# Optimization experiments

Measured on AMD Instinct MI355X. Metric: run time of the kernel, lower is better.

The kernel has to match this reference:

```python
import jax, jax.numpy as jnp
import numpy as np


def setup_inputs() -> dict:
    key = jax.random.key(0)
    ks = jax.random.split(key, 12)
    L, B, T, E, H = 8, 256, 8, 1024, 1024
    w_scale = 1.0 / np.sqrt(E + H)  # keep gates out of saturation (mimics Linear init scale)
    inp = {
        "x": jax.random.normal(ks[0], (B, T, E), dtype=jnp.float32),
        "h0": jax.random.normal(ks[1], (L, B, H), dtype=jnp.float32),
        "c0": jax.random.normal(ks[2], (L, B, H), dtype=jnp.float32),
        "Wu": jax.random.normal(ks[3], (L, E + H, H), dtype=jnp.float32) * w_scale,
        "bu": jax.random.normal(ks[4], (L, H), dtype=jnp.float32) * w_scale,
        "Wf": jax.random.normal(ks[5], (L, E + H, H), dtype=jnp.float32) * w_scale,
        "bf": jax.random.normal(ks[6], (L, H), dtype=jnp.float32) * w_scale,
        "Wo": jax.random.normal(ks[7], (L, E + H, H), dtype=jnp.float32) * w_scale,
        "bo": jax.random.normal(ks[8], (L, H), dtype=jnp.float32) * w_scale,
        "Wc": jax.random.normal(ks[9], (L, E + H, H), dtype=jnp.float32) * w_scale,
        "bc": jax.random.normal(ks[10], (L, H), dtype=jnp.float32) * w_scale,
    }
    return inp


def reference(x, h0, c0, Wu, bu, Wf, bf, Wo, bo, Wc, bc):
    # x: [B,T,E]; h0,c0: [L,B,H]; W*: [L,E+H,H]; b*: [L,H]
    # Faithful to source: num_cells layers, time loop over first num_cells steps (T == L here).
    L = h0.shape[0]
    h = jnp.transpose(h0, (1, 0, 2))  # [B,L,H]
    c = jnp.transpose(c0, (1, 0, 2))

    def step(carry, xt):  # xt: [B,E]
        h, c = carry
        inp = xt
        hs, cs = [], []
        for l in range(L):
            zh = jnp.concatenate([inp, h[:, l]], axis=-1)  # [B, E+H]
            u = jax.nn.sigmoid(zh @ Wu[l] + bu[l])
            f = jax.nn.sigmoid(zh @ Wf[l] + bf[l])
            o = jax.nn.sigmoid(zh @ Wo[l] + bo[l])
            c_tilde = jnp.tanh(zh @ Wc[l] + bc[l])
            c_new = f * c[:, l] + u * c_tilde
            h_new = o * jnp.tanh(c_new)
            hs.append(h_new)
            cs.append(c_new)
            inp = h_new
        h = jnp.stack(hs, axis=1)
        c = jnp.stack(cs, axis=1)
        return (h, c), (h_new, c_new)  # emit top-layer h_t, c_t

    (_, _), (hs, cs) = jax.lax.scan(step, (h, c), jnp.transpose(x, (1, 0, 2)))
    hidden_states = jnp.transpose(hs, (1, 0, 2))  # [B,T,H]
    memory_states = jnp.transpose(cs, (1, 0, 2))
    h_t = hidden_states[:, -1:, :]  # [B,1,H], matches torch slice-shape
    c_t = memory_states[:, -1:, :]
    return hidden_states, memory_states, h_t, c_t
```

## Files before the change

kernel.cpp:

```cpp
#include <hip/hip_runtime.h>
#include <hip/hip_bf16.h>

#define B_ 256
#define T_ 8
#define E_ 1024
#define H_ 1024
#define L_ 8
#define KD 2048
#define ND 4096

#define BM 256
#define BN 128
#define BK 64
#define ABYTES 32768
#define BUFBYTES 49152

typedef __bf16 bf16x8 __attribute__((ext_vector_type(8)));
typedef float floatx4 __attribute__((ext_vector_type(4)));

struct bh4 { __hip_bfloat16 x, y, z, w; };

__device__ __forceinline__ float sigm(float x) { return 1.f / (1.f + __expf(-x)); }
__device__ __forceinline__ float tanh_(float x) { return 1.f - 2.f / (__expf(2.f * x) + 1.f); }

__device__ __forceinline__ void async16(const void* g, void* l) {
    __builtin_amdgcn_global_load_lds(
        (const __attribute__((address_space(1))) void*)g,
        (__attribute__((address_space(3))) void*)l, 16, 0, 0);
}

__global__ __launch_bounds__(256) void prep_weights(
    const float* __restrict__ Wu, const float* __restrict__ Wf,
    const float* __restrict__ Wo, const float* __restrict__ Wc,
    __hip_bfloat16* __restrict__ WT)
{
    __shared__ float sm[32][33];
    int bid = blockIdx.x;
    int jt = bid & 31;
    int kt = (bid >> 5) & 63;
    int g  = (bid >> 11) & 3;
    int l  = bid >> 13;
    const float* src = (g == 0) ? Wu : (g == 1) ? Wf : (g == 2) ? Wo : Wc;
    int tid = threadIdx.x;
    int jl = tid & 31;
    int kl0 = tid >> 5;
#pragma unroll
    for (int r = 0; r < 4; ++r) {
        int kl = r * 8 + kl0;
        sm[kl][jl] = src[((size_t)(l * KD + kt * 32 + kl)) * 1024 + jt * 32 + jl];
    }
    __syncthreads();
    int jw = tid >> 3;
    int kc = (tid & 7) * 4;
    bh4 v;
    v.x = __float2bfloat16(sm[kc + 0][jw]);
    v.y = __float2bfloat16(sm[kc + 1][jw]);
    v.z = __float2bfloat16(sm[kc + 2][jw]);
    v.w = __float2bfloat16(sm[kc + 3][jw]);
    size_t n = (size_t)(jt * 32 + jw) * 4 + g;
    *(bh4*)&WT[((size_t)l * ND + n) * KD + kt * 32 + kc] = v;
}

__global__ __launch_bounds__(256) void prep_misc(
    const float* __restrict__ x,  const float* __restrict__ h0,
    const float* __restrict__ c0,
    const float* __restrict__ bu, const float* __restrict__ bfv,
    const float* __restrict__ bo, const float* __restrict__ bc,
    __hip_bfloat16* __restrict__ xbf, __hip_bfloat16* __restrict__ hb0,
    float* __restrict__ cbuf, float* __restrict__ bcat)
{
    size_t i = (size_t)blockIdx.x * 256 + threadIdx.x;
    const size_t NX = (size_t)B_ * T_ * E_;
    const size_t NH = (size_t)L_ * B_ * H_;
    if (i < NX) {
        xbf[i] = __float2bfloat16(x[i]);
    } else if (i < NX + NH) {
        size_t j = i - NX; hb0[j] = __float2bfloat16(h0[j]);
    } else if (i < NX + 2 * NH) {
        size_t j = i - NX - NH; cbuf[j] = c0[j];
    } else if (i < NX + 2 * NH + (size_t)L_ * ND) {
        size_t j = i - NX - 2 * NH;
        int l = (int)(j >> 12); int n = (int)(j & 4095);
        int jj = n >> 2; int g = n & 3;
        const float* bs = (g == 0) ? bu : (g == 1) ? bfv : (g == 2) ? bo : bc;
        bcat[j] = bs[l * 1024 + jj];
    }
}

__global__ __launch_bounds__(512) void lstm_step(
    int d, int tmin,
    const __hip_bfloat16* __restrict__ xbf,
    const __hip_bfloat16* __restrict__ WT,
    const float* __restrict__ bcat,
    __hip_bfloat16* __restrict__ hb0,
    __hip_bfloat16* __restrict__ hb1,
    float* __restrict__ cbuf,
    float* __restrict__ out)
{
    __shared__ __align__(16) char smraw[2][BUFBYTES];

    int cell = blockIdx.x >> 5;
    int nb   = blockIdx.x & 31;
    int t = tmin + cell;
    int l = d - t;

    const __hip_bfloat16* hread  = (t & 1) ? hb1 : hb0;
    __hip_bfloat16*       hwrite = (t & 1) ? hb0 : hb1;

    const __hip_bfloat16* A1; int sA1;
    if (l == 0) { A1 = xbf + (size_t)t * E_;               sA1 = T_ * E_; }
    else        { A1 = hwrite + (size_t)(l - 1) * B_ * H_; sA1 = H_; }
    const __hip_bfloat16* A2 = hread + (size_t)l * B_ * H_;
    const __hip_bfloat16* Bbase = WT + ((size_t)l * ND + (size_t)nb * BN) * KD;

    int tid  = threadIdx.x;
    int lane = tid & 63;
    int wid  = tid >> 6;
    int wm = (wid & 3) * 64;
    int wn = (wid >> 2) * 64;
    int lr   = lane & 15;
    int quad = lane >> 4;

    int srow = tid >> 3;
    int c    = (tid & 7) ^ (srow & 7);
    const __hip_bfloat16* pA1[4];
    const __hip_bfloat16* pA2[4];
    const __hip_bfloat16* pB[2];
#pragma unroll
    for (int s = 0; s < 4; ++s) {
        int row = s * 64 + srow;
        pA1[s] = A1 + (size_t)row * sA1 + c * 8;
        pA2[s] = A2 + (size_t)row * H_ + c * 8 - E_;
    }
#pragma unroll
    for (int s = 0; s < 2; ++s) {
        int row = s * 64 + srow;
        pB[s] = Bbase + (size_t)row * KD + c * 8;
    }
    int ldsWaveOff = wid * 1024;

    auto stage = [&](int k0, int buf) {
        char* dst = smraw[buf];
        bool first = (k0 < E_);
#pragma unroll
        for (int s = 0; s < 4; ++s) {
            const __hip_bfloat16* g = (first ? pA1[s] : pA2[s]) + k0;
            async16(g, dst + s * 8192 + ldsWaveOff);
        }
#pragma unroll
        for (int s = 0; s < 2; ++s) {
            async16(pB[s] + k0, dst + ABYTES + s * 8192 + ldsWaveOff);
        }
    };

    floatx4 acc[4][4];
    floatx4 zero = {0.f, 0.f, 0.f, 0.f};
#pragma unroll
    for (int mi = 0; mi < 4; ++mi)
#pragma unroll
        for (int ni = 0; ni < 4; ++ni) acc[mi][ni] = zero;

    stage(0, 0);
    __syncthreads();

    for (int kt = 0; kt < KD / BK; ++kt) {
        int cur = kt & 1;
        if (kt < KD / BK - 1) stage((kt + 1) * BK, cur ^ 1);

        const __hip_bfloat16* sm = (const __hip_bfloat16*)smraw[cur];
        const __hip_bfloat16* smB = sm + ABYTES / 2;
#pragma unroll
        for (int ks = 0; ks < 2; ++ks) {
            int xo = (((ks * 4 + quad) ^ (lr & 7)) * 8);
            bf16x8 af[4], bfr[4];
#pragma unroll
            for (int mi = 0; mi < 4; ++mi)
                af[mi] = *(const bf16x8*)&sm[(wm + mi * 16 + lr) * 64 + xo];
#pragma unroll
            for (int ni = 0; ni < 4; ++ni)
                bfr[ni] = *(const bf16x8*)&smB[(wn + ni * 16 + lr) * 64 + xo];
#pragma unroll
            for (int mi = 0; mi < 4; ++mi)
#pragma unroll
                for (int ni = 0; ni < 4; ++ni)
                    acc[mi][ni] = __builtin_amdgcn_mfma_f32_16x16x32_bf16(
                        af[mi], bfr[ni], acc[mi][ni], 0, 0, 0);
        }
        __syncthreads();
    }

    float* outH  = out;
    float* outC  = out + (size_t)B_ * T_ * H_;
    float* outHt = out + 2 * (size_t)B_ * T_ * H_;
    float* outCt = outHt + (size_t)B_ * H_;
    auto sC = (float(*)[BN + 4])smraw[0];

    for (int q = 0; q < 4; ++q) {
        __syncthreads();
        if ((wid & 3) == q) {
#pragma unroll
            for (int mi = 0; mi < 4; ++mi)
#pragma unroll
                for (int ni = 0; ni < 4; ++ni)
#pragma unroll
                    for (int r = 0; r < 4; ++r)
                        sC[mi * 16 + quad * 4 + r][wn + ni * 16 + lr] = acc[mi][ni][r];
        }
        __syncthreads();
#pragma unroll
        for (int s = 0; s < 4; ++s) {
            int p = tid + s * 512;
            int r  = p >> 5;
            int jj = p & 31;
            float4 v  = *(float4*)&sC[r][jj * 4];
            float4 bb = *(const float4*)&bcat[(size_t)l * ND + nb * BN + jj * 4];
            float u  = sigm(v.x + bb.x);
            float f  = sigm(v.y + bb.y);
            float o  = sigm(v.z + bb.z);
            float ct = tanh_(v.w + bb.w);
            int b = q * 64 + r;
            int j = nb * 32 + jj;
            size_t ci = ((size_t)l * B_ + b) * H_ + j;
            float cn = f * cbuf[ci] + u * ct;
            cbuf[ci] = cn;
            float hn = o * tanh_(cn);
            hwrite[ci] = __float2bfloat16(hn);
            if (l == L_ - 1) {
                size_t oi = ((size_t)b * T_ + t) * H_ + j;
                outH[oi] = hn;
                outC[oi] = cn;
                if (t == T_ - 1) {
                    outHt[(size_t)b * H_ + j] = hn;
                    outCt[(size_t)b * H_ + j] = cn;
                }
            }
        }
    }
}

extern "C" void kernel_launch(void* const* d_in, const int* in_sizes, int n_in,
                              void* d_out, int out_size, void* d_ws, size_t ws_size,
                              hipStream_t stream)
{
    const float* x   = (const float*)d_in[0];
    const float* h0  = (const float*)d_in[1];
    const float* c0  = (const float*)d_in[2];
    const float* Wu  = (const float*)d_in[3];
    const float* bu  = (const float*)d_in[4];
    const float* Wf  = (const float*)d_in[5];
    const float* bfv = (const float*)d_in[6];
    const float* Wo  = (const float*)d_in[7];
    const float* bo  = (const float*)d_in[8];
    const float* Wc  = (const float*)d_in[9];
    const float* bc  = (const float*)d_in[10];
    float* out = (float*)d_out;

    char* ws = (char*)d_ws;
    __hip_bfloat16* WT   = (__hip_bfloat16*)(ws);
    float*          bcat = (float*)(ws + 134217728);
    __hip_bfloat16* xbf  = (__hip_bfloat16*)(ws + 134348800);
    __hip_bfloat16* hb0  = (__hip_bfloat16*)(ws + 138543104);
    __hip_bfloat16* hb1  = (__hip_bfloat16*)(ws + 142737408);
    float*          cbuf = (float*)(ws + 146931712);

    hipLaunchKernelGGL(prep_weights, dim3(65536), dim3(256), 0, stream,
                       Wu, Wf, Wo, Wc, WT);
    size_t n2 = (size_t)2097152 * 3 + (size_t)L_ * ND;
    hipLaunchKernelGGL(prep_misc, dim3((unsigned)((n2 + 255) / 256)), dim3(256), 0, stream,
                       x, h0, c0, bu, bfv, bo, bc, xbf, hb0, cbuf, bcat);

    for (int dg = 0; dg <= (T_ - 1) + (L_ - 1); ++dg) {
        int tmin = dg > L_ - 1 ? dg - (L_ - 1) : 0;
        int tmax = dg < T_ - 1 ? dg : T_ - 1;
        int nc = tmax - tmin + 1;
        hipLaunchKernelGGL(lstm_step, dim3(nc * 32), dim3(512), 0, stream,
                           dg, tmin, xbf, WT, bcat, hb0, hb1, cbuf, out);
    }
}
```

Measured before the change: 966.3 us.

## Register-staged double-buffer GEMM pipeline and wider tiles in weight prep

The GEMM main loop stops using direct global-to-LDS async loads. It now prefetches two K-tiles ahead into registers, writes them to the alternate LDS buffer after compute, and synchronises with an explicit lgkmcnt wait plus a barrier. This is meant to hide global latency across a full compute phase and drop the per-iteration __syncthreads over vmcnt. Separately, the weight transpose/convert kernel moves to 64x64 tiles with float4 loads and 16-byte bf16 stores, using fewer, larger blocks. The trade-off is higher register pressure (12 uint4 staging registers plus the accumulators) and extra LDS write instructions. The hand-written waitcnt also relies on global loads finishing before the LDS writes that consume them.

```diff
diff --git a/kernel.cpp b/kernel.cpp
--- a/kernel.cpp
+++ b/kernel.cpp
@@ -12,53 +12,52 @@
 #define BM 256
 #define BN 128
 #define BK 64
+#define KT (KD / BK)
 #define ABYTES 32768
 #define BUFBYTES 49152
 
+#define WAITCNT_LGKM0 0xC07F
+
 typedef __bf16 bf16x8 __attribute__((ext_vector_type(8)));
 typedef float floatx4 __attribute__((ext_vector_type(4)));
 
-struct bh4 { __hip_bfloat16 x, y, z, w; };
-
 __device__ __forceinline__ float sigm(float x) { return 1.f / (1.f + __expf(-x)); }
 __device__ __forceinline__ float tanh_(float x) { return 1.f - 2.f / (__expf(2.f * x) + 1.f); }
-
-__device__ __forceinline__ void async16(const void* g, void* l) {
-    __builtin_amdgcn_global_load_lds(
-        (const __attribute__((address_space(1))) void*)g,
-        (__attribute__((address_space(3))) void*)l, 16, 0, 0);
-}
 
 __global__ __launch_bounds__(256) void prep_weights(
     const float* __restrict__ Wu, const float* __restrict__ Wf,
     const float* __restrict__ Wo, const float* __restrict__ Wc,
     __hip_bfloat16* __restrict__ WT)
 {
-    __shared__ float sm[32][33];
+    __shared__ float sm[64][65];
     int bid = blockIdx.x;
-    int jt = bid & 31;
-    int kt = (bid >> 5) & 63;
-    int g  = (bid >> 11) & 3;
-    int l  = bid >> 13;
+    int jt = bid & 15;
+    int kt = (bid >> 4) & 31;
+    int g  = (bid >> 9) & 3;
+    int l  = bid >> 11;
     const float* src = (g == 0) ? Wu : (g == 1) ? Wf : (g == 2) ? Wo : Wc;
     int tid = threadIdx.x;
-    int jl = tid & 31;
-    int kl0 = tid >> 5;
-#pragma unroll
-    for (int r = 0; r < 4; ++r) {
-        int kl = r * 8 + kl0;
-        sm[kl][jl] = src[((size_t)(l * KD + kt * 32 + kl)) * 1024 + jt * 32 + jl];
+    int cr = tid >> 4;
+    int cc = (tid & 15) * 4;
+    const float* base = src + ((size_t)(l * KD + kt * 64)) * 1024 + jt * 64;
+#pragma unroll
+    for (int p = 0; p < 4; ++p) {
+        int kr = p * 16 + cr;
+        float4 v = *(const float4*)(base + (size_t)kr * 1024 + cc);
+        sm[kr][cc] = v.x; sm[kr][cc + 1] = v.y; sm[kr][cc + 2] = v.z; sm[kr][cc + 3] = v.w;
     }
     __syncthreads();
-    int jw = tid >> 3;
-    int kc = (tid & 7) * 4;
-    bh4 v;
-    v.x = __float2bfloat16(sm[kc + 0][jw]);
-    v.y = __float2bfloat16(sm[kc + 1][jw]);
-    v.z = __float2bfloat16(sm[kc + 2][jw]);
-    v.w = __float2bfloat16(sm[kc + 3][jw]);
-    size_t n = (size_t)(jt * 32 + jw) * 4 + g;
-    *(bh4*)&WT[((size_t)l * ND + n) * KD + kt * 32 + kc] = v;
+    int kc8 = (tid & 7) * 8;
+    int jr0 = tid >> 3;
+#pragma unroll
+    for (int p = 0; p < 2; ++p) {
+        int jr = p * 32 + jr0;
+        __hip_bfloat16 tmp[8];
+#pragma unroll
+        for (int i = 0; i < 8; ++i) tmp[i] = __float2bfloat16(sm[kc8 + i][jr]);
+        size_t n = (size_t)(jt * 64 + jr) * 4 + g;
+        *(uint4*)&WT[((size_t)l * ND + n) * KD + kt * 64 + kc8] = *(uint4*)tmp;
+    }
 }
 
 __global__ __launch_bounds__(256) void prep_misc(
@@ -137,20 +136,25 @@
         int row = s * 64 + srow;
         pB[s] = Bbase + (size_t)row * KD + c * 8;
     }
-    int ldsWaveOff = wid * 1024;
-
-    auto stage = [&](int k0, int buf) {
+    int ldsOff = wid * 1024 + lane * 16;
+
+    auto loadT = [&](int k0, uint4* ra, uint4* rb) {
+        bool first = (k0 < E_);
+#pragma unroll
+        for (int s = 0; s < 4; ++s)
+            ra[s] = *(const uint4*)((first ? pA1[s] : pA2[s]) + k0);
+#pragma unroll
+        for (int s = 0; s < 2; ++s)
+            rb[s] = *(const uint4*)(pB[s] + k0);
+    };
+    auto writeT = [&](int buf, const uint4* ra, const uint4* rb) {
         char* dst = smraw[buf];
-        bool first = (k0 < E_);
-#pragma unroll
-        for (int s = 0; s < 4; ++s) {
-            const __hip_bfloat16* g = (first ? pA1[s] : pA2[s]) + k0;
-            async16(g, dst + s * 8192 + ldsWaveOff);
-        }
-#pragma unroll
-        for (int s = 0; s < 2; ++s) {
-            async16(pB[s] + k0, dst + ABYTES + s * 8192 + ldsWaveOff);
-        }
+#pragma unroll
+        for (int s = 0; s < 4; ++s)
+            *(uint4*)(dst + s * 8192 + ldsOff) = ra[s];
+#pragma unroll
+        for (int s = 0; s < 2; ++s)
+            *(uint4*)(dst + ABYTES + s * 8192 + ldsOff) = rb[s];
     };
 
     floatx4 acc[4][4];
@@ -160,14 +164,8 @@
 #pragma unroll
         for (int ni = 0; ni < 4; ++ni) acc[mi][ni] = zero;
 
-    stage(0, 0);
-    __syncthreads();
-
-    for (int kt = 0; kt < KD / BK; ++kt) {
-        int cur = kt & 1;
-        if (kt < KD / BK - 1) stage((kt + 1) * BK, cur ^ 1);
-
-        const __hip_bfloat16* sm = (const __hip_bfloat16*)smraw[cur];
+    auto compute = [&](const char* buf) {
+        const __hip_bfloat16* sm  = (const __hip_bfloat16*)buf;
         const __hip_bfloat16* smB = sm + ABYTES / 2;
 #pragma unroll
         for (int ks = 0; ks < 2; ++ks) {
@@ -186,7 +184,27 @@
                     acc[mi][ni] = __builtin_amdgcn_mfma_f32_16x16x32_bf16(
                         af[mi], bfr[ni], acc[mi][ni], 0, 0, 0);
         }
-        __syncthreads();
+    };
+
+    uint4 rA[2][4], rB[2][2];
+    loadT(0, rA[0], rB[0]);
+    writeT(0, rA[0], rB[0]);
+    loadT(BK, rA[1], rB[1]);
+    __builtin_amdgcn_s_waitcnt(WAITCNT_LGKM0);
+    __builtin_amdgcn_s_barrier();
+    asm volatile("" ::: "memory");
+
+    for (int kt = 0; kt < KT; ++kt) {
+        int cur = kt & 1;
+        compute(smraw[cur]);
+        if (kt < KT - 1) {
+            writeT(cur ^ 1, rA[(kt + 1) & 1], rB[(kt + 1) & 1]);
+            if (kt < KT - 2)
+                loadT((kt + 2) * BK, rA[kt & 1], rB[kt & 1]);
+        }
+        __builtin_amdgcn_s_waitcnt(WAITCNT_LGKM0);
+        __builtin_amdgcn_s_barrier();
+        asm volatile("" ::: "memory");
     }
 
     float* outH  = out;
@@ -263,7 +281,7 @@
     __hip_bfloat16* hb1  = (__hip_bfloat16*)(ws + 142737408);
     float*          cbuf = (float*)(ws + 146931712);
 
-    hipLaunchKernelGGL(prep_weights, dim3(65536), dim3(256), 0, stream,
+    hipLaunchKernelGGL(prep_weights, dim3(16384), dim3(256), 0, stream,
                        Wu, Wf, Wo, Wc, WT);
     size_t n2 = (size_t)2097152 * 3 + (size_t)L_ * ND;
     hipLaunchKernelGGL(prep_misc, dim3((unsigned)((n2 + 255) / 256)), dim3(256), 0, stream,
```

Measured after the change: 1.755 ms. 81.6% more time.
